# Kernel tuning notes

Measured on AMD Instinct MI355X. Metric: run time of the kernel, lower is better.

The kernel has to match this reference:

```python
import jax, jax.numpy as jnp
import numpy as np

NUM_GROUPS = 32
EPS = 1e-6


def group_norm(x, gamma, beta):
    # x: (B, C, H, W)
    B, C, H, W = x.shape
    g = x.reshape(B, NUM_GROUPS, C // NUM_GROUPS, H, W)
    mean = g.mean(axis=(2, 3, 4), keepdims=True)
    var = g.var(axis=(2, 3, 4), keepdims=True)
    g = (g - mean) / jnp.sqrt(var + EPS)
    g = g.reshape(B, C, H, W)
    return g * gamma[None, :, None, None] + beta[None, :, None, None]


def nin(x, W, b):
    # 1x1 linear projection over channel dim
    return jnp.einsum('bchw,cd->bdhw', x, W) + b[None, :, None, None]


def setup_inputs() -> dict:
    key = jax.random.key(0)
    ks = jax.random.split(key, 8)
    B, C, H, W = 32, 512, 32, 32
    lim = np.sqrt(3 * 0.1 / C)  # NIN init_scale=0.1 uniform limit
    return {
        'x': jax.random.normal(ks[0], (B, C, H, W), jnp.float32),
        'gamma': jnp.ones((C,), jnp.float32),
        'beta': jnp.zeros((C,), jnp.float32),
        'Wq': jax.random.uniform(ks[1], (C, C), jnp.float32, -lim, lim),
        'bq': jnp.zeros((C,), jnp.float32),
        'Wk': jax.random.uniform(ks[2], (C, C), jnp.float32, -lim, lim),
        'bk': jnp.zeros((C,), jnp.float32),
        'Wv': jax.random.uniform(ks[3], (C, C), jnp.float32, -lim, lim),
        'bv': jnp.zeros((C,), jnp.float32),
        'Wp': jax.random.normal(ks[4], (C, C), jnp.float32) * 1e-5,  # init_scale=0.0 -> ~0
        'bp': jnp.zeros((C,), jnp.float32),
    }


def reference(x, gamma, beta, Wq, bq, Wk, bk, Wv, bv, Wp, bp):
    B, C, H, W = x.shape
    h = group_norm(x, gamma, beta)
    q = nin(h, Wq, bq)
    k = nin(h, Wk, bk)
    v = nin(h, Wv, bv)
    # full (HW)x(HW) attention weights, as the original materializes
    w = jnp.einsum('bchw,bcHW->bhwHW', q, k) * (C ** -0.5)
    w = w.reshape(B, H, W, H * W)
    w = jax.nn.softmax(w, axis=-1)
    w = w.reshape(B, H, W, H, W)
    h_out = jnp.einsum('bhwHW,bcHW->bchw', w, v)
    h_out = nin(h_out, Wp, bp)
    return x + h_out
```

## Files before the change

### kernel.cpp

```cpp
#include <hip/hip_runtime.h>
#include <hip/hip_bf16.h>
#include <math.h>

typedef __attribute__((ext_vector_type(8))) short bf16x8;
typedef __attribute__((ext_vector_type(4))) float f32x4;

typedef const __attribute__((address_space(1))) unsigned int guint;
typedef __attribute__((address_space(3))) unsigned int luint;

static __device__ __forceinline__ short f2bf(float f) {
    union { float f; unsigned u; } a; a.f = f;
    unsigned r = 0x7FFFu + ((a.u >> 16) & 1u);
    return (short)((a.u + r) >> 16);
}
static __device__ __forceinline__ float bf2f(short s) {
    union { unsigned u; float f; } a;
    a.u = ((unsigned)(unsigned short)s) << 16;
    return a.f;
}

__global__ __launch_bounds__(256)
void transpose_w(const float* __restrict__ w0, const float* __restrict__ w1,
                 const float* __restrict__ w2, const float* __restrict__ w3,
                 short* __restrict__ outT, float qscale)
{
    __shared__ float ld[32][33];
    const float* W = (blockIdx.z == 0) ? w0 : (blockIdx.z == 1) ? w1
                   : (blockIdx.z == 2) ? w2 : w3;
    const float sc = (blockIdx.z == 0) ? qscale : 1.f;
    short* O = outT + (long long)blockIdx.z * 512 * 512;
    const int tx = threadIdx.x & 31, ty = threadIdx.x >> 5;
    const int c0 = blockIdx.y * 32, d0 = blockIdx.x * 32;
#pragma unroll
    for (int r = 0; r < 4; ++r)
        ld[ty + 8 * r][tx] = W[(long long)(c0 + ty + 8 * r) * 512 + d0 + tx];
    __syncthreads();
#pragma unroll
    for (int r = 0; r < 4; ++r)
        O[(long long)(d0 + ty + 8 * r) * 512 + c0 + tx] = f2bf(ld[tx][ty + 8 * r] * sc);
}

__global__ __launch_bounds__(256)
void concat_bias(const float* __restrict__ bq, const float* __restrict__ bk,
                 float* __restrict__ bqk, float qscale)
{
    int i = blockIdx.x * 256 + threadIdx.x;
    bqk[i] = (i < 512) ? bq[i] * qscale : bk[i - 512];
}

__global__ __launch_bounds__(256)
void gn_stats(const float* __restrict__ x, float2* __restrict__ stats)
{
    const int bg = blockIdx.x;
    const float4* p = reinterpret_cast<const float4*>(x + (long long)bg * 16384);
    float s = 0.f, ss = 0.f;
    for (int i = threadIdx.x; i < 4096; i += 256) {
        float4 v = p[i];
        s  += v.x + v.y + v.z + v.w;
        ss += v.x * v.x + v.y * v.y + v.z * v.z + v.w * v.w;
    }
    __shared__ float rs[256], rss[256];
    rs[threadIdx.x] = s; rss[threadIdx.x] = ss;
    __syncthreads();
    for (int o = 128; o > 0; o >>= 1) {
        if (threadIdx.x < o) { rs[threadIdx.x] += rs[threadIdx.x + o];
                               rss[threadIdx.x] += rss[threadIdx.x + o]; }
        __syncthreads();
    }
    if (threadIdx.x == 0) {
        float mean = rs[0] * (1.f / 16384.f);
        float var  = rss[0] * (1.f / 16384.f) - mean * mean;
        stats[bg] = make_float2(mean, rsqrtf(var + 1e-6f));
    }
}

__global__ __launch_bounds__(256)
void gn_apply_t(const float* __restrict__ x, const float2* __restrict__ stats,
                const float* __restrict__ gamma, const float* __restrict__ beta,
                short* __restrict__ hn)
{
    __shared__ short lds[32 * 520];
    const int t = threadIdx.x;
    const int s0 = blockIdx.x * 32;
    const int b  = blockIdx.y;
#pragma unroll
    for (int i = 0; i < 16; ++i) {
        int qi = t + 256 * i;
        int c = qi >> 3, sc = qi & 7;
        float4 v = *reinterpret_cast<const float4*>(
            x + ((long long)(b * 512 + c)) * 1024 + s0 + sc * 4);
        float2 st = stats[b * 32 + (c >> 4)];
        float ga = gamma[c], be = beta[c];
        float m = st.x, r = st.y;
        lds[(sc * 4 + 0) * 520 + c] = f2bf((v.x - m) * r * ga + be);
        lds[(sc * 4 + 1) * 520 + c] = f2bf((v.y - m) * r * ga + be);
        lds[(sc * 4 + 2) * 520 + c] = f2bf((v.z - m) * r * ga + be);
        lds[(sc * 4 + 3) * 520 + c] = f2bf((v.w - m) * r * ga + be);
    }
    __syncthreads();
#pragma unroll
    for (int i = 0; i < 8; ++i) {
        int p = t + 256 * i;
        int s = p >> 6, j = p & 63;
        float4 v = *reinterpret_cast<const float4*>(&lds[s * 520 + j * 8]);
        *reinterpret_cast<float4*>(
            hn + ((long long)(b * 1024 + s0 + s)) * 512 + j * 8) = v;
    }
}

template<int BIAS_M, int BIAS_N, int RESID, int EXPRS, int DIVROW4>
__global__ __launch_bounds__(512, 1)
void nt_gemm(const short* __restrict__ A, const short* __restrict__ B,
             void* __restrict__ Cv,
             const float* __restrict__ biasM, const float* __restrict__ biasN,
             const float* __restrict__ resid, float* __restrict__ rs,
             float scale, int K, int lda, int ldb, int ldc,
             long long sA, long long sB, long long sC,
             int tilesM, int tilesPerBatch)
{
    __shared__ short lsA[2][2][128 * 64];
    __shared__ short lsB[2][2][128 * 64];

    const int id = blockIdx.x;
    const int chunk = gridDim.x >> 3;
    const int gid = (id & 7) * chunk + (id >> 3);
    const int bz = gid / tilesPerBatch;
    const int tt = gid - bz * tilesPerBatch;
    const int m0 = (tt % tilesM) * 256;
    const int n0 = (tt / tilesM) * 256;

    const int t = threadIdx.x;
    const int lane = t & 63;
    const int w = t >> 6;
    const int wrs = w >> 1;
    const int wcs = w & 1;
    const int lr16 = lane & 15, lkg = lane >> 4;
    const int sw = lr16 & 7;

    const int srow = t >> 3;
    const int scol = ((t & 7) ^ (srow & 7)) * 8;
    const short* gA = A + (long long)bz * sA + (long long)(m0 + srow) * lda + scol;
    const short* gB = B + (long long)bz * sB + (long long)(n0 + srow) * ldb + scol;

    f32x4 acc[4][2][4];
#pragma unroll
    for (int q = 0; q < 4; ++q)
#pragma unroll
        for (int i = 0; i < 2; ++i)
#pragma unroll
            for (int j = 0; j < 4; ++j) acc[q][i][j] = (f32x4){0.f, 0.f, 0.f, 0.f};

    const int nk = K >> 6;

#define STAGE_A(buf, h, kt)                                                    \
    {                                                                          \
        _Pragma("unroll")                                                      \
        for (int c = 0; c < 2; ++c)                                            \
            __builtin_amdgcn_global_load_lds(                                  \
                (guint*)(gA + (long long)((h) * 128 + 64 * c) * lda + (kt) * 64), \
                (luint*)&lsA[buf][h][t * 8 + 4096 * c], 16, 0, 0);             \
    }
#define STAGE_B(buf, h, kt)                                                    \
    {                                                                          \
        _Pragma("unroll")                                                      \
        for (int c = 0; c < 2; ++c)                                            \
            __builtin_amdgcn_global_load_lds(                                  \
                (guint*)(gB + (long long)((h) * 128 + 64 * c) * ldb + (kt) * 64), \
                (luint*)&lsB[buf][h][t * 8 + 4096 * c], 16, 0, 0);             \
    }

#define LDA_HALF(dst, buf, h)                                                  \
    _Pragma("unroll")                                                          \
    for (int mi2 = 0; mi2 < 2; ++mi2)                                          \
        _Pragma("unroll")                                                      \
        for (int ks = 0; ks < 2; ++ks)                                         \
            dst[mi2][ks] = *reinterpret_cast<const bf16x8*>(                   \
                &lsA[buf][h][(wrs * 32 + mi2 * 16 + lr16) * 64 +               \
                             (((ks * 4 + lkg) ^ sw) * 8)]);
#define LDB_HALF(dst, buf, h)                                                  \
    _Pragma("unroll")                                                          \
    for (int ni = 0; ni < 4; ++ni)                                             \
        _Pragma("unroll")                                                      \
        for (int ks = 0; ks < 2; ++ks)                                         \
            dst[ni][ks] = *reinterpret_cast<const bf16x8*>(                    \
                &lsB[buf][h][(wcs * 64 + ni * 16 + lr16) * 64 +                \
                             (((ks * 4 + lkg) ^ sw) * 8)]);

#define MFMAQ(q, Af, Bf)                                                       \
    _Pragma("unroll")                                                          \
    for (int ks = 0; ks < 2; ++ks)                                             \
        _Pragma("unroll")                                                      \
        for (int mi2 = 0; mi2 < 2; ++mi2)                                      \
            _Pragma("unroll")                                                  \
            for (int ni = 0; ni < 4; ++ni)                                     \
                acc[q][mi2][ni] = __builtin_amdgcn_mfma_f32_16x16x32_bf16(     \
                    Af[mi2][ks], Bf[ni][ks], acc[q][mi2][ni], 0, 0, 0);

#define PH_END(N)                                                              \
    asm volatile("s_waitcnt vmcnt(" #N ")" ::: "memory");                      \
    __builtin_amdgcn_s_barrier();                                              \
    __builtin_amdgcn_sched_barrier(0)

#define FRAME(b, kt)                                                           \
    {                                                                          \
        bf16x8 a0[2][2], a1[2][2], b0f[4][2], b1f[4][2];                       \
           \
        LDB_HALF(b0f, b, 0)                                                    \
        LDA_HALF(a0, b, 0)                                                     \
        LDB_HALF(b1f, b, 1)                                                    \
        STAGE_B((b) ^ 1, 0, (kt) + 1);                                         \
        STAGE_B((b) ^ 1, 1, (kt) + 1);                                         \
        STAGE_A((b) ^ 1, 0, (kt) + 1);                                         \
        MFMAQ(0, a0, b0f)                                                      \
        MFMAQ(1, a0, b1f)                                                      \
        PH_END(6);                                                             \
              \
        LDA_HALF(a1, b, 1)                                                     \
        STAGE_A((b) ^ 1, 1, (kt) + 1);                                         \
        MFMAQ(2, a1, b0f)                                                      \
        MFMAQ(3, a1, b1f)                                                      \
        PH_END(2);                                                             \
    }

    STAGE_B(0, 0, 0); STAGE_B(0, 1, 0); STAGE_A(0, 0, 0);
    STAGE_A(0, 1, 0);
    PH_END(2);

    for (int kt = 0; kt < nk; kt += 2) {
        FRAME(0, kt)
        FRAME(1, kt + 1)
    }
#undef STAGE_A
#undef STAGE_B
#undef LDA_HALF
#undef LDB_HALF
#undef MFMAQ
#undef PH_END
#undef FRAME

    float psum[2][2][4];
    if (EXPRS) {
#pragma unroll
        for (int ah = 0; ah < 2; ++ah)
#pragma unroll
            for (int mi2 = 0; mi2 < 2; ++mi2)
#pragma unroll
                for (int j = 0; j < 4; ++j) psum[ah][mi2][j] = 0.f;
    }
#pragma unroll
    for (int ah = 0; ah < 2; ++ah) {
#pragma unroll
        for (int bh = 0; bh < 2; ++bh) {
#pragma unroll
            for (int mi2 = 0; mi2 < 2; ++mi2) {
                float addm[4], mul[4];
#pragma unroll
                for (int j = 0; j < 4; ++j) {
                    const int rrow = m0 + ah * 128 + wrs * 32 + mi2 * 16 + lkg * 4 + j;
                    addm[j] = BIAS_M ? biasM[rrow] : 0.f;
                    if (DIVROW4) {
                        const float* r4 = rs + (long long)bz * 4096 + rrow;
                        mul[j] = 1.f / (r4[0] + r4[1024] + r4[2048] + r4[3072]);
                    } else mul[j] = 1.f;
                }
#pragma unroll
                for (int ni = 0; ni < 4; ++ni) {
                    const int col = n0 + bh * 128 + wcs * 64 + ni * 16 + lr16;
                    float bn = BIAS_N ? biasN[col] : 0.f;
#pragma unroll
                    for (int j = 0; j < 4; ++j) {
                        const int rrow = m0 + ah * 128 + wrs * 32 + mi2 * 16 + lkg * 4 + j;
                        float v2 = acc[ah * 2 + bh][mi2][ni][j] + addm[j] + bn;
                        v2 *= scale;
                        if (EXPRS) { v2 = __expf(v2 - 8.f); psum[ah][mi2][j] += v2; }
                        if (DIVROW4) v2 *= mul[j];
                        const long long idx = (long long)rrow * ldc + col;
                        if (RESID) {
                            float* Cf = (float*)Cv + (long long)bz * sC;
                            Cf[idx] = v2 + resid[(long long)bz * sC + idx];
                        } else {
                            short* Cs = (short*)Cv + (long long)bz * sC;
                            Cs[idx] = f2bf(v2);
                        }
                    }
                }
            }
        }
    }
    if (EXPRS) {
#pragma unroll
        for (int ah = 0; ah < 2; ++ah)
#pragma unroll
            for (int mi2 = 0; mi2 < 2; ++mi2)
#pragma unroll
                for (int j = 0; j < 4; ++j) {
                    float v = psum[ah][mi2][j];
                    v += __shfl_xor(v, 1); v += __shfl_xor(v, 2);
                    v += __shfl_xor(v, 4); v += __shfl_xor(v, 8);
                    psum[ah][mi2][j] = v;
                }
        float* scr = (float*)&lsA[1][0][0];
        __syncthreads();
        if (lr16 == 0) {
#pragma unroll
            for (int ah = 0; ah < 2; ++ah)
#pragma unroll
                for (int mi2 = 0; mi2 < 2; ++mi2)
#pragma unroll
                    for (int j = 0; j < 4; ++j)
                        scr[wcs * 256 + ah * 128 + wrs * 32 + mi2 * 16 + lkg * 4 + j]
                            = psum[ah][mi2][j];
        }
        __syncthreads();
        if (t < 256)
            rs[(long long)bz * 4096 + (n0 >> 8) * 1024 + m0 + t]
                = scr[t] + scr[256 + t];
    }
}

extern "C" void kernel_launch(void* const* d_in, const int* in_sizes, int n_in,
                              void* d_out, int out_size, void* d_ws, size_t ws_size,
                              hipStream_t stream)
{
    (void)in_sizes; (void)n_in; (void)out_size; (void)ws_size;
    const float* x     = (const float*)d_in[0];
    const float* gamma = (const float*)d_in[1];
    const float* beta  = (const float*)d_in[2];
    const float* Wq = (const float*)d_in[3];
    const float* bq = (const float*)d_in[4];
    const float* Wk = (const float*)d_in[5];
    const float* bk = (const float*)d_in[6];
    const float* Wv = (const float*)d_in[7];
    const float* bv = (const float*)d_in[8];
    const float* Wp = (const float*)d_in[9];
    const float* bp = (const float*)d_in[10];
    float* out = (float*)d_out;

    char* ws = (char*)d_ws;
    short*  expS = (short*)ws;
    short*  hn   = (short*)ws;
    short*  qkb  = (short*)(ws + (64LL << 20));
    short*  vbuf = (short*)(ws + (128LL << 20));
    short*  wT   = (short*)(ws + (160LL << 20));
    float2* stats = (float2*)(ws + (162LL << 20));
    float*  bqk   = (float*)(ws + (162LL << 20) + (16 << 10));
    float*  rs4   = (float*)(ws + (162LL << 20) + (32 << 10));
    short*  ho    = qkb;

    const short* WqkT = wT;
    const short* WvT  = wT + 2 * 512 * 512;
    const short* WpT  = wT + 3 * 512 * 512;

    const float qscale = 0.044194173824159216f;

    transpose_w<<<dim3(16, 16, 4), 256, 0, stream>>>(Wq, Wk, Wv, Wp, wT, qscale);
    concat_bias<<<dim3(4), 256, 0, stream>>>(bq, bk, bqk, qscale);
    gn_stats<<<dim3(1024), 256, 0, stream>>>(x, stats);
    gn_apply_t<<<dim3(32, 32), 256, 0, stream>>>(x, stats, gamma, beta, hn);

    nt_gemm<0, 1, 0, 0, 0><<<512, 512, 0, stream>>>(
        hn, WqkT, qkb, nullptr, bqk, nullptr, nullptr, 1.f,
        512, 512, 512, 1024, 1024 * 512, 0, 1024LL * 1024, 4, 16);
    nt_gemm<1, 0, 0, 0, 0><<<256, 512, 0, stream>>>(
        WvT, hn, vbuf, bv, nullptr, nullptr, nullptr, 1.f,
        512, 512, 512, 1024, 0, 1024 * 512, 512 * 1024, 2, 8);
    nt_gemm<0, 0, 0, 1, 0><<<512, 512, 0, stream>>>(
        qkb, qkb + 512, expS, nullptr, nullptr, nullptr, rs4, 1.f,
        512, 1024, 1024, 1024, 1024LL * 1024, 1024LL * 1024, 1024LL * 1024, 4, 16);
    nt_gemm<0, 0, 0, 0, 1><<<256, 512, 0, stream>>>(
        expS, vbuf, ho, nullptr, nullptr, nullptr, rs4, 1.f,
        1024, 1024, 1024, 512, 1024LL * 1024, 512 * 1024, 1024 * 512, 4, 8);
    nt_gemm<1, 0, 1, 0, 0><<<256, 512, 0, stream>>>(
        WpT, ho, out, bp, nullptr, x, nullptr, 1.f,
        512, 512, 512, 1024, 0, 1024 * 512, 512LL * 1024, 2, 8);
}
```

Measured before the change: 205.9 us.

## Fuse group-norm stats and apply into one kernel with group-blocked hn layout

Merges gn_stats and gn_apply_t into a single kernel that caches each (batch, group) slab of x in 64KB of LDS, reduces mean and variance, then writes normalized bf16 output. The output uses a group-blocked layout [b][g][s][16 channels] instead of [b][s][512], and the GEMM loaders gain HN_A/HN_B template paths that address this layout. This removes the second read of x and one launch. In exchange it uses heavy LDS per block, which limits occupancy, and the K-stride jumps make GEMM loads less contiguous.

```diff
diff --git a/kernel.cpp b/kernel.cpp
--- a/kernel.cpp
+++ b/kernel.cpp
@@ -49,66 +49,60 @@
 }
 
 __global__ __launch_bounds__(256)
-void gn_stats(const float* __restrict__ x, float2* __restrict__ stats)
-{
+void gn_fused(const float* __restrict__ x, const float* __restrict__ gamma,
+              const float* __restrict__ beta, short* __restrict__ hn)
+{
+    __shared__ float xs[16 * 1024];
+    __shared__ float red[256];
     const int bg = blockIdx.x;
-    const float4* p = reinterpret_cast<const float4*>(x + (long long)bg * 16384);
+    const int g  = bg & 31;
+    const int t  = threadIdx.x;
+    const float4* px = reinterpret_cast<const float4*>(x + (long long)bg * 16384);
     float s = 0.f, ss = 0.f;
-    for (int i = threadIdx.x; i < 4096; i += 256) {
-        float4 v = p[i];
+#pragma unroll
+    for (int i = 0; i < 16; ++i) {
+        float4 v = px[t + 256 * i];
+        reinterpret_cast<float4*>(xs)[t + 256 * i] = v;
         s  += v.x + v.y + v.z + v.w;
         ss += v.x * v.x + v.y * v.y + v.z * v.z + v.w * v.w;
     }
-    __shared__ float rs[256], rss[256];
-    rs[threadIdx.x] = s; rss[threadIdx.x] = ss;
+    red[t] = s; __syncthreads();
+    for (int o = 128; o > 0; o >>= 1) {
+        if (t < o) red[t] += red[t + o];
+        __syncthreads();
+    }
+    const float mean = red[0] * (1.f / 16384.f);
     __syncthreads();
+    red[t] = ss; __syncthreads();
     for (int o = 128; o > 0; o >>= 1) {
-        if (threadIdx.x < o) { rs[threadIdx.x] += rs[threadIdx.x + o];
-                               rss[threadIdx.x] += rss[threadIdx.x + o]; }
+        if (t < o) red[t] += red[t + o];
         __syncthreads();
     }
-    if (threadIdx.x == 0) {
-        float mean = rs[0] * (1.f / 16384.f);
-        float var  = rss[0] * (1.f / 16384.f) - mean * mean;
-        stats[bg] = make_float2(mean, rsqrtf(var + 1e-6f));
-    }
-}
-
-__global__ __launch_bounds__(256)
-void gn_apply_t(const float* __restrict__ x, const float2* __restrict__ stats,
-                const float* __restrict__ gamma, const float* __restrict__ beta,
-                short* __restrict__ hn)
-{
-    __shared__ short lds[32 * 520];
-    const int t = threadIdx.x;
-    const int s0 = blockIdx.x * 32;
-    const int b  = blockIdx.y;
-#pragma unroll
-    for (int i = 0; i < 16; ++i) {
-        int qi = t + 256 * i;
-        int c = qi >> 3, sc = qi & 7;
-        float4 v = *reinterpret_cast<const float4*>(
-            x + ((long long)(b * 512 + c)) * 1024 + s0 + sc * 4);
-        float2 st = stats[b * 32 + (c >> 4)];
-        float ga = gamma[c], be = beta[c];
-        float m = st.x, r = st.y;
-        lds[(sc * 4 + 0) * 520 + c] = f2bf((v.x - m) * r * ga + be);
-        lds[(sc * 4 + 1) * 520 + c] = f2bf((v.y - m) * r * ga + be);
-        lds[(sc * 4 + 2) * 520 + c] = f2bf((v.z - m) * r * ga + be);
-        lds[(sc * 4 + 3) * 520 + c] = f2bf((v.w - m) * r * ga + be);
-    }
-    __syncthreads();
-#pragma unroll
-    for (int i = 0; i < 8; ++i) {
-        int p = t + 256 * i;
-        int s = p >> 6, j = p & 63;
-        float4 v = *reinterpret_cast<const float4*>(&lds[s * 520 + j * 8]);
-        *reinterpret_cast<float4*>(
-            hn + ((long long)(b * 1024 + s0 + s)) * 512 + j * 8) = v;
-    }
-}
-
-template<int BIAS_M, int BIAS_N, int RESID, int EXPRS, int DIVROW4>
+    const float var  = red[0] * (1.f / 16384.f) - mean * mean;
+    const float rstd = rsqrtf(var + 1e-6f);
+
+    const int half = t & 1;
+    float ga[8], be[8];
+#pragma unroll
+    for (int cc = 0; cc < 8; ++cc) {
+        ga[cc] = gamma[g * 16 + half * 8 + cc];
+        be[cc] = beta[g * 16 + half * 8 + cc];
+    }
+    short* out = hn + (long long)bg * 16384;
+#pragma unroll
+    for (int it = 0; it < 8; ++it) {
+        const int sidx = it * 128 + (t >> 1);
+        bf16x8 o;
+#pragma unroll
+        for (int cc = 0; cc < 8; ++cc) {
+            float v = xs[(half * 8 + cc) * 1024 + sidx];
+            o[cc] = f2bf((v - mean) * rstd * ga[cc] + be[cc]);
+        }
+        *reinterpret_cast<bf16x8*>(out + sidx * 16 + half * 8) = o;
+    }
+}
+
+template<int BIAS_M, int BIAS_N, int RESID, int EXPRS, int DIVROW4, int HN_A, int HN_B>
 __global__ __launch_bounds__(512, 1)
 void nt_gemm(const short* __restrict__ A, const short* __restrict__ B,
              void* __restrict__ Cv,
@@ -138,9 +132,27 @@
     const int sw = lr16 & 7;
 
     const int srow = t >> 3;
-    const int scol = ((t & 7) ^ (srow & 7)) * 8;
-    const short* gA = A + (long long)bz * sA + (long long)(m0 + srow) * lda + scol;
-    const short* gB = B + (long long)bz * sB + (long long)(n0 + srow) * ldb + scol;
+    const int jch  = (t & 7) ^ (srow & 7);
+    const int scol = jch * 8;
+
+    const short* gA; int rsA, ktA;
+    if (HN_A) {
+        gA = A + ((long long)bz * 32 + (jch >> 1)) * 16384
+               + (long long)(m0 + srow) * 16 + (jch & 1) * 8;
+        rsA = 16; ktA = 65536;
+    } else {
+        gA = A + (long long)bz * sA + (long long)(m0 + srow) * lda + scol;
+        rsA = lda; ktA = 64;
+    }
+    const short* gB; int rsB, ktB;
+    if (HN_B) {
+        gB = B + ((long long)bz * 32 + (jch >> 1)) * 16384
+               + (long long)(n0 + srow) * 16 + (jch & 1) * 8;
+        rsB = 16; ktB = 65536;
+    } else {
+        gB = B + (long long)bz * sB + (long long)(n0 + srow) * ldb + scol;
+        rsB = ldb; ktB = 64;
+    }
 
     f32x4 acc[4][2][4];
 #pragma unroll
@@ -157,7 +169,8 @@
         _Pragma("unroll")                                                      \
         for (int c = 0; c < 2; ++c)                                            \
             __builtin_amdgcn_global_load_lds(                                  \
-                (guint*)(gA + (long long)((h) * 128 + 64 * c) * lda + (kt) * 64), \
+                (guint*)(gA + (long long)(kt) * ktA                            \
+                            + (long long)((h) * 128 + 64 * c) * rsA),          \
                 (luint*)&lsA[buf][h][t * 8 + 4096 * c], 16, 0, 0);             \
     }
 #define STAGE_B(buf, h, kt)                                                    \
@@ -165,7 +178,8 @@
         _Pragma("unroll")                                                      \
         for (int c = 0; c < 2; ++c)                                            \
             __builtin_amdgcn_global_load_lds(                                  \
-                (guint*)(gB + (long long)((h) * 128 + 64 * c) * ldb + (kt) * 64), \
+                (guint*)(gB + (long long)(kt) * ktB                            \
+                            + (long long)((h) * 128 + 64 * c) * rsB),          \
                 (luint*)&lsB[buf][h][t * 8 + 4096 * c], 16, 0, 0);             \
     }
 
@@ -342,10 +356,9 @@
     short*  qkb  = (short*)(ws + (64LL << 20));
     short*  vbuf = (short*)(ws + (128LL << 20));
     short*  wT   = (short*)(ws + (160LL << 20));
-    float2* stats = (float2*)(ws + (162LL << 20));
-    float*  bqk   = (float*)(ws + (162LL << 20) + (16 << 10));
-    float*  rs4   = (float*)(ws + (162LL << 20) + (32 << 10));
-    short*  ho    = qkb;
+    float*  bqk  = (float*)(ws + (162LL << 20) + (16 << 10));
+    float*  rs4  = (float*)(ws + (162LL << 20) + (32 << 10));
+    short*  ho   = qkb;
 
     const short* WqkT = wT;
     const short* WvT  = wT + 2 * 512 * 512;
@@ -355,22 +368,21 @@
 
     transpose_w<<<dim3(16, 16, 4), 256, 0, stream>>>(Wq, Wk, Wv, Wp, wT, qscale);
     concat_bias<<<dim3(4), 256, 0, stream>>>(bq, bk, bqk, qscale);
-    gn_stats<<<dim3(1024), 256, 0, stream>>>(x, stats);
-    gn_apply_t<<<dim3(32, 32), 256, 0, stream>>>(x, stats, gamma, beta, hn);
-
-    nt_gemm<0, 1, 0, 0, 0><<<512, 512, 0, stream>>>(
+    gn_fused<<<dim3(1024), 256, 0, stream>>>(x, gamma, beta, hn);
+
+    nt_gemm<0, 1, 0, 0, 0, 1, 0><<<512, 512, 0, stream>>>(
         hn, WqkT, qkb, nullptr, bqk, nullptr, nullptr, 1.f,
-        512, 512, 512, 1024, 1024 * 512, 0, 1024LL * 1024, 4, 16);
-    nt_gemm<1, 0, 0, 0, 0><<<256, 512, 0, stream>>>(
+        512, 512, 512, 1024, 0, 0, 1024LL * 1024, 4, 16);
+    nt_gemm<1, 0, 0, 0, 0, 0, 1><<<256, 512, 0, stream>>>(
         WvT, hn, vbuf, bv, nullptr, nullptr, nullptr, 1.f,
-        512, 512, 512, 1024, 0, 1024 * 512, 512 * 1024, 2, 8);
-    nt_gemm<0, 0, 0, 1, 0><<<512, 512, 0, stream>>>(
+        512, 512, 512, 1024, 0, 0, 512 * 1024, 2, 8);
+    nt_gemm<0, 0, 0, 1, 0, 0, 0><<<512, 512, 0, stream>>>(
         qkb, qkb + 512, expS, nullptr, nullptr, nullptr, rs4, 1.f,
         512, 1024, 1024, 1024, 1024LL * 1024, 1024LL * 1024, 1024LL * 1024, 4, 16);
-    nt_gemm<0, 0, 0, 0, 1><<<256, 512, 0, stream>>>(
+    nt_gemm<0, 0, 0, 0, 1, 0, 0><<<256, 512, 0, stream>>>(
         expS, vbuf, ho, nullptr, nullptr, nullptr, rs4, 1.f,
         1024, 1024, 1024, 512, 1024LL * 1024, 512 * 1024, 1024 * 512, 4, 8);
-    nt_gemm<1, 0, 1, 0, 0><<<256, 512, 0, stream>>>(
+    nt_gemm<1, 0, 1, 0, 0, 0, 0><<<256, 512, 0, stream>>>(
         WpT, ho, out, bp, nullptr, x, nullptr, 1.f,
         512, 512, 512, 1024, 0, 1024 * 512, 512LL * 1024, 2, 8);
 }
```

Result: no change. 201.9 us (-1.9%).
